# Kernel optimization log

Measured on AMD Instinct MI355X. Metric: run time of the kernel, lower is better.

Reference implementation:

```python
import jax, jax.numpy as jnp
import numpy as np

D_MODEL = 1024
N_HEADS = 16
D_K = D_MODEL // N_HEADS


def setup_inputs() -> dict:
    key = jax.random.key(0)
    k1, k2, k3, k4, k5 = jax.random.split(key, 5)
    B, S = 2, 2048
    scale = 1.0 / np.sqrt(D_MODEL)
    return {
        "query": jax.random.normal(k1, (B, S, D_MODEL), dtype=jnp.float32),
        "mask": jnp.ones((B, S, S), dtype=jnp.int32),
        "W_qkv": jax.random.normal(k2, (D_MODEL, 3 * D_MODEL), dtype=jnp.float32) * scale,
        "b_qkv": jax.random.normal(k3, (3 * D_MODEL,), dtype=jnp.float32) * 0.02,
        "W_out": jax.random.normal(k4, (D_MODEL, D_MODEL), dtype=jnp.float32) * scale,
        "b_out": jax.random.normal(k5, (D_MODEL,), dtype=jnp.float32) * 0.02,
    }


def reference(query, mask, W_qkv, b_qkv, W_out, b_out):
    B, S, _ = query.shape
    # fused QKV projection (all from query, matching the torch module)
    qkv = query @ W_qkv + b_qkv                      # [B, S, 3*D]
    q, k, v = jnp.split(qkv, 3, axis=-1)
    # [B, H, S, d_k]
    q = q.reshape(B, S, N_HEADS, D_K).transpose(0, 2, 1, 3)
    k = k.reshape(B, S, N_HEADS, D_K).transpose(0, 2, 1, 3)
    v = v.reshape(B, S, N_HEADS, D_K).transpose(0, 2, 1, 3)
    # scaled dot-product attention with explicit scores
    scores = jnp.einsum("bhqd,bhkd->bhqk", q, k) / jnp.sqrt(jnp.float32(D_K))
    m = mask[:, None, :, :]                           # [B, 1, S, S] broadcast over heads
    scores = jnp.where(m == 0, jnp.float32(-1e9), scores)
    attn = jax.nn.softmax(scores, axis=-1)           # dropout p=0 in eval -> identity
    ctx = jnp.einsum("bhqk,bhkd->bhqd", attn, v)     # [B, H, S, d_k]
    ctx = ctx.transpose(0, 2, 1, 3).reshape(B, S, D_MODEL)
    return ctx @ W_out + b_out
```

## Files before the change

kernel.cpp:

```cpp
#include <hip/hip_runtime.h>
#include <stdint.h>
#include <stddef.h>

#define S_LEN 2048
#define NB    2
#define DM    1024
#define NH    16
#define DKH   64
#define NTOK  4096
#define QKV_N 3072
#define QSCALE 0.18033688f

typedef __attribute__((ext_vector_type(4))) float floatx4;
using half2v = __attribute__((ext_vector_type(2))) _Float16;
using half4v = __attribute__((ext_vector_type(4))) _Float16;
using half8v = __attribute__((ext_vector_type(8))) _Float16;
using fp16x2 = __attribute__((ext_vector_type(2))) __fp16;

#if __has_builtin(__builtin_amdgcn_exp2f)
#define EXP2F __builtin_amdgcn_exp2f
#else
#define EXP2F exp2f
#endif

#define WAITCNT_VM4() asm volatile("s_waitcnt vmcnt(4)" ::: "memory")
#define WAITCNT_VM0() asm volatile("s_waitcnt vmcnt(0)" ::: "memory")
#define BARRIER_RAW() asm volatile("s_barrier" ::: "memory")

__device__ __forceinline__ void glds16(const void* g, void* l) {
    __builtin_amdgcn_global_load_lds((const __attribute__((address_space(1))) void*)g,
                                     (__attribute__((address_space(3))) void*)l,
                                     16, 0, 0);
}

__global__ __launch_bounds__(256) void prep_kernel(const float* __restrict__ query,
                                                   _Float16* __restrict__ qh,
                                                   const float* __restrict__ Wqkv,
                                                   _Float16* __restrict__ wqt,
                                                   const float* __restrict__ Wout,
                                                   _Float16* __restrict__ wot,
                                                   const int* __restrict__ mask,
                                                   int* __restrict__ flag) {
    __shared__ float tbuf[32][33];
    constexpr int CAST_B = NTOK * DM / 4 / 256;
    constexpr int TQ_B   = (QKV_N / 32) * (DM / 32);
    constexpr int TO_B   = (DM / 32) * (DM / 32);
    const int bid = blockIdx.x;

    if (bid < CAST_B) {
        int i = bid * 256 + threadIdx.x;
        float4 v = ((const float4*)query)[i];
        half4v o = {(_Float16)v.x, (_Float16)v.y, (_Float16)v.z, (_Float16)v.w};
        ((half4v*)qh)[i] = o;
    } else if (bid < CAST_B + TQ_B + TO_B) {
        const float* in; _Float16* out; int C, t;
        if (bid < CAST_B + TQ_B) { t = bid - CAST_B;        in = Wqkv; out = wqt; C = QKV_N; }
        else                     { t = bid - CAST_B - TQ_B; in = Wout; out = wot; C = DM;    }
        const int R = DM;
        int c0 = (t % (C / 32)) * 32, r0 = (t / (C / 32)) * 32;
        int x = threadIdx.x & 31, y0 = threadIdx.x >> 5;
        #pragma unroll
        for (int k = 0; k < 4; ++k) {
            int y = y0 + k * 8;
            tbuf[y][x] = in[(size_t)(r0 + y) * C + c0 + x];
        }
        __syncthreads();
        #pragma unroll
        for (int k = 0; k < 4; ++k) {
            int y = y0 + k * 8;
            out[(size_t)(c0 + y) * R + r0 + x] = (_Float16)tbuf[x][y];
        }
    } else {
        int i = (bid - CAST_B - TQ_B - TO_B) * 256 + threadIdx.x;
        int4 v = ((const int4*)mask)[i];
        if ((v.x == 0) | (v.y == 0) | (v.z == 0) | (v.w == 0)) *flag = 0;
    }
}

template <int FINAL, int BN>
__global__ __launch_bounds__(256) void gemm_bt_kernel(const _Float16* __restrict__ A,
                                                      const _Float16* __restrict__ Bt,
                                                      const float* __restrict__ bias,
                                                      float* __restrict__ Cf,
                                                      _Float16* __restrict__ Ch,
                                                      _Float16* __restrict__ Vt,
                                                      int M, int N, int K) {
    constexpr int NJ = BN / 32;
    __shared__ _Float16 As[128 * 64];
    __shared__ _Float16 Bs[BN * 64];

    const int nt = blockIdx.x, mt = blockIdx.y;
    const int tid = threadIdx.x, wave = tid >> 6, lane = tid & 63;
    const int quad = lane >> 4, l16 = lane & 15;
    const int wm = wave >> 1, wn = wave & 1;

    floatx4 acc[4][NJ];
    #pragma unroll
    for (int i = 0; i < 4; ++i)
        #pragma unroll
        for (int j = 0; j < NJ; ++j)
            #pragma unroll
            for (int r = 0; r < 4; ++r) acc[i][j][r] = 0.0f;

    const _Float16* Ab = A + (size_t)mt * 128 * K;
    const _Float16* Bb = Bt + (size_t)nt * BN * K;

    for (int kt = 0; kt < K; kt += 64) {
        #pragma unroll
        for (int p = 0; p < 4; ++p) {
            int slot = p * 256 + wave * 64 + lane;
            int row = slot >> 3, cc = slot & 7, c = cc ^ (row & 7);
            glds16(Ab + (size_t)row * K + kt + c * 8, As + (size_t)(p * 256 + wave * 64) * 8);
        }
        #pragma unroll
        for (int p = 0; p < BN / 32; ++p) {
            int slot = p * 256 + wave * 64 + lane;
            int row = slot >> 3, cc = slot & 7, c = cc ^ (row & 7);
            glds16(Bb + (size_t)row * K + kt + c * 8, Bs + (size_t)(p * 256 + wave * 64) * 8);
        }
        __syncthreads();

        #pragma unroll
        for (int kk = 0; kk < 2; ++kk) {
            half8v af[4], bfr[NJ];
            #pragma unroll
            for (int i = 0; i < 4; ++i) {
                int row = wm * 64 + i * 16 + l16;
                int c = (kk * 4 + quad) ^ (row & 7);
                af[i] = *(const half8v*)(As + row * 64 + c * 8);
            }
            #pragma unroll
            for (int j = 0; j < NJ; ++j) {
                int row = wn * (BN / 2) + j * 16 + l16;
                int c = (kk * 4 + quad) ^ (row & 7);
                bfr[j] = *(const half8v*)(Bs + row * 64 + c * 8);
            }
            #pragma unroll
            for (int i = 0; i < 4; ++i)
                #pragma unroll
                for (int j = 0; j < NJ; ++j)
                    acc[i][j] = __builtin_amdgcn_mfma_f32_16x16x32_f16(af[i], bfr[j], acc[i][j], 0, 0, 0);
        }
        __syncthreads();
    }

    #pragma unroll
    for (int j = 0; j < NJ; ++j) {
        int n = nt * BN + wn * (BN / 2) + j * 16 + l16;
        float bv = bias[n];
        #pragma unroll
        for (int i = 0; i < 4; ++i) {
            int m0 = mt * 128 + wm * 64 + i * 16 + quad * 4;
            float v[4];
            #pragma unroll
            for (int r = 0; r < 4; ++r) v[r] = acc[i][j][r] + bv;
            if (FINAL) {
                #pragma unroll
                for (int r = 0; r < 4; ++r) Cf[(size_t)(m0 + r) * N + n] = v[r];
            } else {
                if (n < DM) {
                    #pragma unroll
                    for (int r = 0; r < 4; ++r) v[r] *= QSCALE;
                }
                if (n < 2 * DM) {
                    #pragma unroll
                    for (int r = 0; r < 4; ++r)
                        Ch[(size_t)(m0 + r) * QKV_N + n] = (_Float16)v[r];
                } else {
                    int bb = m0 >> 11, s = m0 & (S_LEN - 1);
                    half4v t = {(_Float16)v[0], (_Float16)v[1], (_Float16)v[2], (_Float16)v[3]};
                    *(half4v*)(Vt + ((size_t)bb * (NH * DKH) + (n - 2 * DM)) * S_LEN + s) = t;
                }
            }
        }
    }
}

__global__ __launch_bounds__(512, 4) void flash_kernel(const _Float16* __restrict__ qkv,
                                                       const _Float16* __restrict__ vt,
                                                       const int* __restrict__ mask,
                                                       const int* __restrict__ flag,
                                                       _Float16* __restrict__ ctx) {
    __shared__ _Float16 Ks[2][2][64 * 64];
    __shared__ _Float16 Vs[2][2][64 * 64];

    const int bh = blockIdx.x, qt = blockIdx.y;
    const int b = bh >> 4, h = bh & 15;
    const int tid = threadIdx.x, wave = tid >> 6, lane = tid & 63;
    const int quad = lane >> 4, l16 = lane & 15;
    const int grp = wave >> 2;
    const int w4 = wave & 3;
    const int allones = (*flag != 0);

    const _Float16* qrow0 = qkv + (size_t)(b * S_LEN + qt * 128 + w4 * 32 + l16) * QKV_N + h * DKH;
    const _Float16* qrow1 = qrow0 + (size_t)16 * QKV_N;
    half8v qa0 = *(const half8v*)(qrow0 + quad * 8);
    half8v qa1 = *(const half8v*)(qrow0 + 32 + quad * 8);
    half8v qb0 = *(const half8v*)(qrow1 + quad * 8);
    half8v qb1 = *(const half8v*)(qrow1 + 32 + quad * 8);
    WAITCNT_VM0();

    const _Float16* kbase = qkv + (size_t)(b * S_LEN + grp * 1024) * QKV_N + DM + h * DKH;
    const _Float16* vbase = vt + (size_t)(b * NH + h) * DKH * S_LEN + grp * 1024;

    auto stage = [&](int buf, int kt) {
        #pragma unroll
        for (int p = 0; p < 2; ++p) {
            int slot = p * 256 + w4 * 64 + lane;
            int row = slot >> 3, cc = slot & 7, c = cc ^ (row & 7);
            glds16(kbase + (size_t)(kt * 64 + row) * QKV_N + c * 8,
                   &Ks[grp][buf][(p * 256 + w4 * 64) * 8]);
        }
        #pragma unroll
        for (int p = 0; p < 2; ++p) {
            int slot = p * 256 + w4 * 64 + lane;
            int row = slot >> 3, cc = slot & 7, c = cc ^ (row & 7);
            glds16(vbase + (size_t)row * S_LEN + kt * 64 + c * 8,
                   &Vs[grp][buf][(p * 256 + w4 * 64) * 8]);
        }
    };

    floatx4 oa[4], ob[4];
    #pragma unroll
    for (int c = 0; c < 4; ++c)
        #pragma unroll
        for (int r = 0; r < 4; ++r) { oa[c][r] = 0.0f; ob[c][r] = 0.0f; }
    float lsa = 0.0f, lsb = 0.0f;

    stage(0, 0);

    for (int kt = 0; kt < 16; ++kt) {
        const int cur = kt & 1;
        if (kt < 15) {
            stage(cur ^ 1, kt + 1);
            WAITCNT_VM4();
        } else {
            WAITCNT_VM0();
        }
        BARRIER_RAW();

        const _Float16* Ksb = Ks[grp][cur];
        const _Float16* Vsb = Vs[grp][cur];

        half4v pa[4], pb[4];
        #pragma unroll
        for (int j = 0; j < 4; ++j) {
            int rowk = j * 16 + l16;
            half8v a0 = *(const half8v*)(Ksb + rowk * 64 + ((quad) ^ (rowk & 7)) * 8);
            half8v a1 = *(const half8v*)(Ksb + rowk * 64 + ((4 + quad) ^ (rowk & 7)) * 8);
            floatx4 za, zb;
            #pragma unroll
            for (int r = 0; r < 4; ++r) { za[r] = 0.0f; zb[r] = 0.0f; }
            za = __builtin_amdgcn_mfma_f32_16x16x32_f16(a0, qa0, za, 0, 0, 0);
            za = __builtin_amdgcn_mfma_f32_16x16x32_f16(a1, qa1, za, 0, 0, 0);
            zb = __builtin_amdgcn_mfma_f32_16x16x32_f16(a0, qb0, zb, 0, 0, 0);
            zb = __builtin_amdgcn_mfma_f32_16x16x32_f16(a1, qb1, zb, 0, 0, 0);

            if (!allones) {
                for (int r = 0; r < 4; ++r) {
                    int s = grp * 1024 + kt * 64 + j * 16 + quad * 4 + r;
                    int qA = qt * 128 + w4 * 32 + l16;
                    if (mask[((size_t)b * S_LEN + qA) * S_LEN + s] == 0) za[r] = -1e9f;
                    if (mask[((size_t)b * S_LEN + qA + 16) * S_LEN + s] == 0) zb[r] = -1e9f;
                }
            }

            float p0 = EXP2F(za[0]), p1 = EXP2F(za[1]), p2 = EXP2F(za[2]), p3 = EXP2F(za[3]);
            lsa += (p0 + p1) + (p2 + p3);
            fp16x2 lo = __builtin_amdgcn_cvt_pkrtz(p0, p1);
            fp16x2 hi = __builtin_amdgcn_cvt_pkrtz(p2, p3);
            half2v lo2 = __builtin_bit_cast(half2v, lo);
            half2v hi2 = __builtin_bit_cast(half2v, hi);
            half4v pka = {lo2.x, lo2.y, hi2.x, hi2.y};
            pa[j] = pka;

            p0 = EXP2F(zb[0]); p1 = EXP2F(zb[1]); p2 = EXP2F(zb[2]); p3 = EXP2F(zb[3]);
            lsb += (p0 + p1) + (p2 + p3);
            lo = __builtin_amdgcn_cvt_pkrtz(p0, p1);
            hi = __builtin_amdgcn_cvt_pkrtz(p2, p3);
            lo2 = __builtin_bit_cast(half2v, lo);
            hi2 = __builtin_bit_cast(half2v, hi);
            half4v pkb = {lo2.x, lo2.y, hi2.x, hi2.y};
            pb[j] = pkb;
        }

        #pragma unroll
        for (int j = 0; j < 4; ++j) {
            int g2 = 2 * j + (quad >> 1);
            #pragma unroll
            for (int c = 0; c < 4; ++c) {
                int rowv = c * 16 + l16;
                half4v bv = *(const half4v*)(Vsb + rowv * 64 + ((g2 ^ (rowv & 7)) * 8) + (quad & 1) * 4);
                oa[c] = __builtin_amdgcn_mfma_f32_16x16x16f16(pa[j], bv, oa[c], 0, 0, 0);
                ob[c] = __builtin_amdgcn_mfma_f32_16x16x16f16(pb[j], bv, ob[c], 0, 0, 0);
            }
        }

        if (kt < 15) BARRIER_RAW();
    }

    __syncthreads();
    float* obuf = (float*)&Ks[0][0][0];
    float* lbuf = (float*)&Vs[0][0][0];
    if (grp == 1) {
        #pragma unroll
        for (int c = 0; c < 4; ++c)
            #pragma unroll
            for (int r = 0; r < 4; ++r) {
                obuf[(w4 * 32 + (c * 4 + r)) * 64 + lane]      = oa[c][r];
                obuf[(w4 * 32 + 16 + (c * 4 + r)) * 64 + lane] = ob[c][r];
            }
        lbuf[(w4 * 2 + 0) * 64 + lane] = lsa;
        lbuf[(w4 * 2 + 1) * 64 + lane] = lsb;
    }
    __syncthreads();
    if (grp == 0) {
        #pragma unroll
        for (int c = 0; c < 4; ++c)
            #pragma unroll
            for (int r = 0; r < 4; ++r) {
                oa[c][r] += obuf[(w4 * 32 + (c * 4 + r)) * 64 + lane];
                ob[c][r] += obuf[(w4 * 32 + 16 + (c * 4 + r)) * 64 + lane];
            }
        lsa += lbuf[(w4 * 2 + 0) * 64 + lane];
        lsb += lbuf[(w4 * 2 + 1) * 64 + lane];

        lsa += __shfl_xor(lsa, 16); lsa += __shfl_xor(lsa, 32);
        lsb += __shfl_xor(lsb, 16); lsb += __shfl_xor(lsb, 32);
        float lia[4], lib[4];
        #pragma unroll
        for (int r = 0; r < 4; ++r) {
            int src = (lane & 48) | ((lane >> 4) * 4 + r);
            lia[r] = 1.0f / __shfl(lsa, src);
            lib[r] = 1.0f / __shfl(lsb, src);
        }

        #pragma unroll
        for (int c = 0; c < 4; ++c)
            #pragma unroll
            for (int r = 0; r < 4; ++r) {
                int qA = qt * 128 + w4 * 32 + quad * 4 + r;
                int col = h * DKH + c * 16 + l16;
                ctx[(size_t)(b * S_LEN + qA) * DM + col]      = (_Float16)(oa[c][r] * lia[r]);
                ctx[(size_t)(b * S_LEN + qA + 16) * DM + col] = (_Float16)(ob[c][r] * lib[r]);
            }
    }
}

extern "C" void kernel_launch(void* const* d_in, const int* in_sizes, int n_in,
                              void* d_out, int out_size, void* d_ws, size_t ws_size,
                              hipStream_t stream) {
    const float* query = (const float*)d_in[0];
    const int*   mask  = (const int*)d_in[1];
    const float* W_qkv = (const float*)d_in[2];
    const float* b_qkv = (const float*)d_in[3];
    const float* W_out = (const float*)d_in[4];
    const float* b_out = (const float*)d_in[5];
    float* out = (float*)d_out;

    char* w = (char*)d_ws;
    _Float16* qh   = (_Float16*)w;  w += (size_t)NTOK * DM * 2;
    _Float16* wqt  = (_Float16*)w;  w += (size_t)QKV_N * DM * 2;
    _Float16* wot  = (_Float16*)w;  w += (size_t)DM * DM * 2;
    _Float16* qkvh = (_Float16*)w;  w += (size_t)NTOK * QKV_N * 2;
    _Float16* vt   = (_Float16*)w;  w += (size_t)NB * NH * DKH * S_LEN * 2;
    int*      flag = (int*)w;
    _Float16* ctxh = qh;

    hipMemsetAsync(flag, 1, 4, stream);

    constexpr int PREP_BLOCKS = (NTOK * DM / 4 / 256)
                              + (QKV_N / 32) * (DM / 32)
                              + (DM / 32) * (DM / 32)
                              + (NB * S_LEN * S_LEN / 4 / 256);
    prep_kernel<<<PREP_BLOCKS, 256, 0, stream>>>(query, qh, W_qkv, wqt, W_out, wot, mask, flag);

    gemm_bt_kernel<0, 128><<<dim3(QKV_N / 128, NTOK / 128), 256, 0, stream>>>(
        qh, wqt, b_qkv, nullptr, qkvh, vt, NTOK, QKV_N, DM);

    flash_kernel<<<dim3(NB * NH, S_LEN / 128), 512, 0, stream>>>(qkvh, vt, mask, flag, ctxh);

    gemm_bt_kernel<1, 64><<<dim3(DM / 64, NTOK / 128), 256, 0, stream>>>(
        ctxh, wot, b_out, out, nullptr, nullptr, NTOK, DM, DM);
}
```

Baseline: 211.2 us.

## Double-buffer GEMM K-tiles and stage attention output through LDS for coalesced stores

The GEMM kernel now uses two 32-wide K buffers in LDS and issues async global-to-LDS loads for the next tile before computing the current one, synchronising with vmcnt waits and raw barriers instead of two full __syncthreads per 64-wide step. It also sets launch_bounds occupancy to 4 blocks. The attention epilogue writes the normalized fp16 context into LDS first and then stores it to global memory as 16-byte coalesced rows instead of scattered 2-byte stores. The aim is to overlap memory latency with MFMA work and cut store transactions, at the cost of more barriers per K and possible register pressure from the occupancy hint.

New measurement: 218.4 us. +3.4%, slower.

```diff
diff --git a/kernel.cpp b/kernel.cpp
--- a/kernel.cpp
+++ b/kernel.cpp
@@ -24,6 +24,7 @@
 #endif
 
 #define WAITCNT_VM4() asm volatile("s_waitcnt vmcnt(4)" ::: "memory")
+#define WAITCNT_VM3() asm volatile("s_waitcnt vmcnt(3)" ::: "memory")
 #define WAITCNT_VM0() asm volatile("s_waitcnt vmcnt(0)" ::: "memory")
 #define BARRIER_RAW() asm volatile("s_barrier" ::: "memory")
 
@@ -78,16 +79,16 @@
 }
 
 template <int FINAL, int BN>
-__global__ __launch_bounds__(256) void gemm_bt_kernel(const _Float16* __restrict__ A,
-                                                      const _Float16* __restrict__ Bt,
-                                                      const float* __restrict__ bias,
-                                                      float* __restrict__ Cf,
-                                                      _Float16* __restrict__ Ch,
-                                                      _Float16* __restrict__ Vt,
-                                                      int M, int N, int K) {
+__global__ __launch_bounds__(256, 4) void gemm_bt_kernel(const _Float16* __restrict__ A,
+                                                         const _Float16* __restrict__ Bt,
+                                                         const float* __restrict__ bias,
+                                                         float* __restrict__ Cf,
+                                                         _Float16* __restrict__ Ch,
+                                                         _Float16* __restrict__ Vt,
+                                                         int M, int N, int K) {
     constexpr int NJ = BN / 32;
-    __shared__ _Float16 As[128 * 64];
-    __shared__ _Float16 Bs[BN * 64];
+    __shared__ _Float16 As[2][128 * 32];
+    __shared__ _Float16 Bs[2][BN * 32];
 
     const int nt = blockIdx.x, mt = blockIdx.y;
     const int tid = threadIdx.x, wave = tid >> 6, lane = tid & 63;
@@ -105,43 +106,53 @@
     const _Float16* Ab = A + (size_t)mt * 128 * K;
     const _Float16* Bb = Bt + (size_t)nt * BN * K;
 
-    for (int kt = 0; kt < K; kt += 64) {
-        #pragma unroll
-        for (int p = 0; p < 4; ++p) {
+    auto stage = [&](int buf, int kt) {
+        #pragma unroll
+        for (int p = 0; p < 2; ++p) {
             int slot = p * 256 + wave * 64 + lane;
-            int row = slot >> 3, cc = slot & 7, c = cc ^ (row & 7);
-            glds16(Ab + (size_t)row * K + kt + c * 8, As + (size_t)(p * 256 + wave * 64) * 8);
-        }
-        #pragma unroll
-        for (int p = 0; p < BN / 32; ++p) {
+            int row = slot >> 2, cc = slot & 3, c = cc ^ (row & 3);
+            glds16(Ab + (size_t)row * K + kt * 32 + c * 8, &As[buf][(p * 256 + wave * 64) * 8]);
+        }
+        #pragma unroll
+        for (int p = 0; p < BN / 64; ++p) {
             int slot = p * 256 + wave * 64 + lane;
-            int row = slot >> 3, cc = slot & 7, c = cc ^ (row & 7);
-            glds16(Bb + (size_t)row * K + kt + c * 8, Bs + (size_t)(p * 256 + wave * 64) * 8);
-        }
-        __syncthreads();
-
-        #pragma unroll
-        for (int kk = 0; kk < 2; ++kk) {
-            half8v af[4], bfr[NJ];
-            #pragma unroll
-            for (int i = 0; i < 4; ++i) {
-                int row = wm * 64 + i * 16 + l16;
-                int c = (kk * 4 + quad) ^ (row & 7);
-                af[i] = *(const half8v*)(As + row * 64 + c * 8);
-            }
-            #pragma unroll
-            for (int j = 0; j < NJ; ++j) {
-                int row = wn * (BN / 2) + j * 16 + l16;
-                int c = (kk * 4 + quad) ^ (row & 7);
-                bfr[j] = *(const half8v*)(Bs + row * 64 + c * 8);
-            }
-            #pragma unroll
-            for (int i = 0; i < 4; ++i)
-                #pragma unroll
-                for (int j = 0; j < NJ; ++j)
-                    acc[i][j] = __builtin_amdgcn_mfma_f32_16x16x32_f16(af[i], bfr[j], acc[i][j], 0, 0, 0);
-        }
-        __syncthreads();
+            int row = slot >> 2, cc = slot & 3, c = cc ^ (row & 3);
+            glds16(Bb + (size_t)row * K + kt * 32 + c * 8, &Bs[buf][(p * 256 + wave * 64) * 8]);
+        }
+    };
+
+    stage(0, 0);
+    const int NKT = K / 32;
+    for (int kt = 0; kt < NKT; ++kt) {
+        const int cur = kt & 1;
+        if (kt < NKT - 1) {
+            stage(cur ^ 1, kt + 1);
+            if constexpr (BN == 128) { WAITCNT_VM4(); } else { WAITCNT_VM3(); }
+        } else {
+            WAITCNT_VM0();
+        }
+        BARRIER_RAW();
+
+        half8v af[4], bfr[NJ];
+        #pragma unroll
+        for (int i = 0; i < 4; ++i) {
+            int row = wm * 64 + i * 16 + l16;
+            int c = quad ^ (row & 3);
+            af[i] = *(const half8v*)(&As[cur][row * 32 + c * 8]);
+        }
+        #pragma unroll
+        for (int j = 0; j < NJ; ++j) {
+            int row = wn * (BN / 2) + j * 16 + l16;
+            int c = quad ^ (row & 3);
+            bfr[j] = *(const half8v*)(&Bs[cur][row * 32 + c * 8]);
+        }
+        #pragma unroll
+        for (int i = 0; i < 4; ++i)
+            #pragma unroll
+            for (int j = 0; j < NJ; ++j)
+                acc[i][j] = __builtin_amdgcn_mfma_f32_16x16x32_f16(af[i], bfr[j], acc[i][j], 0, 0, 0);
+
+        if (kt < NKT - 1) BARRIER_RAW();
     }
 
     #pragma unroll
@@ -302,6 +313,7 @@
     __syncthreads();
     float* obuf = (float*)&Ks[0][0][0];
     float* lbuf = (float*)&Vs[0][0][0];
+    _Float16* st = (_Float16*)&Vs[0][0][0] + 2048;
     if (grp == 1) {
         #pragma unroll
         for (int c = 0; c < 4; ++c)
@@ -339,11 +351,18 @@
         for (int c = 0; c < 4; ++c)
             #pragma unroll
             for (int r = 0; r < 4; ++r) {
-                int qA = qt * 128 + w4 * 32 + quad * 4 + r;
-                int col = h * DKH + c * 16 + l16;
-                ctx[(size_t)(b * S_LEN + qA) * DM + col]      = (_Float16)(oa[c][r] * lia[r]);
-                ctx[(size_t)(b * S_LEN + qA + 16) * DM + col] = (_Float16)(ob[c][r] * lib[r]);
-            }
+                st[(w4 * 32 + quad * 4 + r) * 64 + c * 16 + l16]      = (_Float16)(oa[c][r] * lia[r]);
+                st[(w4 * 32 + 16 + quad * 4 + r) * 64 + c * 16 + l16] = (_Float16)(ob[c][r] * lib[r]);
+            }
+    }
+    __syncthreads();
+
+    #pragma unroll
+    for (int p = 0; p < 2; ++p) {
+        int cid = p * 512 + tid;
+        int row = cid >> 3, off = (cid & 7) * 8;
+        half8v vv = *(const half8v*)(st + row * 64 + off);
+        *(half8v*)(ctx + (size_t)(b * S_LEN + qt * 128 + row) * DM + h * DKH + off) = vv;
     }
 }
 
```

## Triple-buffer GEMM shared-memory tiles with async prefetch two stages ahead

Applied to the files above, without the earlier changes.

Turns the GEMM k-loop into a three-stage pipeline. global_load_lds copies for tile kt+2 are issued before computing tile kt, and explicit vmcnt waits plus raw barriers replace the load-then-sync pattern, so global memory latency overlaps with MFMA work. The K tile size becomes a template parameter: 32 for the QKV projection and 64 for the output projection. The cost is three times the LDS per block, which may cut occupancy, and more barriers per unit of work in the BK=32 case.

After: 209.6 us. About the same (-0.8%).

```diff
diff --git a/kernel.cpp b/kernel.cpp
--- a/kernel.cpp
+++ b/kernel.cpp
@@ -26,6 +26,15 @@
 #define WAITCNT_VM4() asm volatile("s_waitcnt vmcnt(4)" ::: "memory")
 #define WAITCNT_VM0() asm volatile("s_waitcnt vmcnt(0)" ::: "memory")
 #define BARRIER_RAW() asm volatile("s_barrier" ::: "memory")
+
+template <int N> __device__ __forceinline__ void waitcnt_vm() {
+    if constexpr (N == 0)       asm volatile("s_waitcnt vmcnt(0)" ::: "memory");
+    else if constexpr (N == 4)  asm volatile("s_waitcnt vmcnt(4)" ::: "memory");
+    else if constexpr (N == 6)  asm volatile("s_waitcnt vmcnt(6)" ::: "memory");
+    else if constexpr (N == 8)  asm volatile("s_waitcnt vmcnt(8)" ::: "memory");
+    else if constexpr (N == 12) asm volatile("s_waitcnt vmcnt(12)" ::: "memory");
+    else static_assert(N == 0, "unsupported vmcnt");
+}
 
 __device__ __forceinline__ void glds16(const void* g, void* l) {
     __builtin_amdgcn_global_load_lds((const __attribute__((address_space(1))) void*)g,
@@ -77,7 +86,7 @@
     }
 }
 
-template <int FINAL, int BN>
+template <int FINAL, int BN, int BK>
 __global__ __launch_bounds__(256) void gemm_bt_kernel(const _Float16* __restrict__ A,
                                                       const _Float16* __restrict__ Bt,
                                                       const float* __restrict__ bias,
@@ -85,9 +94,13 @@
                                                       _Float16* __restrict__ Ch,
                                                       _Float16* __restrict__ Vt,
                                                       int M, int N, int K) {
-    constexpr int NJ = BN / 32;
-    __shared__ _Float16 As[128 * 64];
-    __shared__ _Float16 Bs[BN * 64];
+    constexpr int NJ  = BN / 32;
+    constexpr int GR  = BK / 8;
+    constexpr int NKK = BK / 32;
+    constexpr int PA  = 128 * GR / 256;
+    constexpr int PB  = BN * GR / 256;
+    __shared__ _Float16 As[3][128 * BK];
+    __shared__ _Float16 Bs[3][BN * BK];
 
     const int nt = blockIdx.x, mt = blockIdx.y;
     const int tid = threadIdx.x, wave = tid >> 6, lane = tid & 63;
@@ -105,35 +118,53 @@
     const _Float16* Ab = A + (size_t)mt * 128 * K;
     const _Float16* Bb = Bt + (size_t)nt * BN * K;
 
-    for (int kt = 0; kt < K; kt += 64) {
-        #pragma unroll
-        for (int p = 0; p < 4; ++p) {
-            int slot = p * 256 + wave * 64 + lane;
-            int row = slot >> 3, cc = slot & 7, c = cc ^ (row & 7);
-            glds16(Ab + (size_t)row * K + kt + c * 8, As + (size_t)(p * 256 + wave * 64) * 8);
-        }
-        #pragma unroll
-        for (int p = 0; p < BN / 32; ++p) {
-            int slot = p * 256 + wave * 64 + lane;
-            int row = slot >> 3, cc = slot & 7, c = cc ^ (row & 7);
-            glds16(Bb + (size_t)row * K + kt + c * 8, Bs + (size_t)(p * 256 + wave * 64) * 8);
-        }
-        __syncthreads();
-
-        #pragma unroll
-        for (int kk = 0; kk < 2; ++kk) {
+    auto stage = [&](int buf, int kt) {
+        #pragma unroll
+        for (int p = 0; p < PA; ++p) {
+            int slot = p * 256 + tid;
+            int row = slot / GR, cc = slot % GR, c = cc ^ (row & (GR - 1));
+            glds16(Ab + (size_t)row * K + kt * BK + c * 8,
+                   &As[buf][(size_t)(p * 256 + wave * 64) * 8]);
+        }
+        #pragma unroll
+        for (int p = 0; p < PB; ++p) {
+            int slot = p * 256 + tid;
+            int row = slot / GR, cc = slot % GR, c = cc ^ (row & (GR - 1));
+            glds16(Bb + (size_t)row * K + kt * BK + c * 8,
+                   &Bs[buf][(size_t)(p * 256 + wave * 64) * 8]);
+        }
+    };
+
+    const int NKT = K / BK;
+    stage(0, 0);
+    stage(1, 1);
+
+    int cur = 0;
+    for (int kt = 0; kt < NKT; ++kt) {
+        if (kt + 2 < NKT) {
+            stage((kt + 2) % 3, kt + 2);
+            waitcnt_vm<2 * (PA + PB)>();
+        } else if (kt + 2 == NKT) {
+            waitcnt_vm<PA + PB>();
+        } else {
+            waitcnt_vm<0>();
+        }
+        BARRIER_RAW();
+
+        #pragma unroll
+        for (int kk = 0; kk < NKK; ++kk) {
             half8v af[4], bfr[NJ];
             #pragma unroll
             for (int i = 0; i < 4; ++i) {
                 int row = wm * 64 + i * 16 + l16;
-                int c = (kk * 4 + quad) ^ (row & 7);
-                af[i] = *(const half8v*)(As + row * 64 + c * 8);
+                int c = (kk * 4 + quad) ^ (row & (GR - 1));
+                af[i] = *(const half8v*)(&As[cur][row * BK + c * 8]);
             }
             #pragma unroll
             for (int j = 0; j < NJ; ++j) {
                 int row = wn * (BN / 2) + j * 16 + l16;
-                int c = (kk * 4 + quad) ^ (row & 7);
-                bfr[j] = *(const half8v*)(Bs + row * 64 + c * 8);
+                int c = (kk * 4 + quad) ^ (row & (GR - 1));
+                bfr[j] = *(const half8v*)(&Bs[cur][row * BK + c * 8]);
             }
             #pragma unroll
             for (int i = 0; i < 4; ++i)
@@ -141,7 +172,9 @@
                 for (int j = 0; j < NJ; ++j)
                     acc[i][j] = __builtin_amdgcn_mfma_f32_16x16x32_f16(af[i], bfr[j], acc[i][j], 0, 0, 0);
         }
-        __syncthreads();
+
+        if (kt < NKT - 1) BARRIER_RAW();
+        cur = (cur == 2) ? 0 : cur + 1;
     }
 
     #pragma unroll
@@ -375,11 +408,11 @@
                               + (NB * S_LEN * S_LEN / 4 / 256);
     prep_kernel<<<PREP_BLOCKS, 256, 0, stream>>>(query, qh, W_qkv, wqt, W_out, wot, mask, flag);
 
-    gemm_bt_kernel<0, 128><<<dim3(QKV_N / 128, NTOK / 128), 256, 0, stream>>>(
+    gemm_bt_kernel<0, 128, 32><<<dim3(QKV_N / 128, NTOK / 128), 256, 0, stream>>>(
         qh, wqt, b_qkv, nullptr, qkvh, vt, NTOK, QKV_N, DM);
 
     flash_kernel<<<dim3(NB * NH, S_LEN / 128), 512, 0, stream>>>(qkvh, vt, mask, flag, ctxh);
 
-    gemm_bt_kernel<1, 64><<<dim3(DM / 64, NTOK / 128), 256, 0, stream>>>(
+    gemm_bt_kernel<1, 64, 64><<<dim3(DM / 64, NTOK / 128), 256, 0, stream>>>(
         ctxh, wot, b_out, out, nullptr, nullptr, NTOK, DM, DM);
 }
```

## Overlap mask scan and W_out transpose with QKV GEMM via interleaved blocks

Applied to the files above, without the earlier changes.

Moves the mask scan and the W_out transpose/cast out of the prep kernel and into the QKV projection GEMM launch. One in every 13 blocks does a GEMM tile and the other 12 do mask or transpose work, so the memory-bound side work can run alongside the MFMA-bound GEMM. This shortens the critical prep kernel, but the GEMM grid becomes sparse and interleaved, which may change scheduling and cache behavior. The block counts must match exactly: 12 side blocks per GEMM tile times 768 tiles must cover all mask and transpose blocks.

Result: slower. 216.6 us (+2.5%).

```diff
diff --git a/kernel.cpp b/kernel.cpp
--- a/kernel.cpp
+++ b/kernel.cpp
@@ -36,15 +36,9 @@
 __global__ __launch_bounds__(256) void prep_kernel(const float* __restrict__ query,
                                                    _Float16* __restrict__ qh,
                                                    const float* __restrict__ Wqkv,
-                                                   _Float16* __restrict__ wqt,
-                                                   const float* __restrict__ Wout,
-                                                   _Float16* __restrict__ wot,
-                                                   const int* __restrict__ mask,
-                                                   int* __restrict__ flag) {
+                                                   _Float16* __restrict__ wqt) {
     __shared__ float tbuf[32][33];
     constexpr int CAST_B = NTOK * DM / 4 / 256;
-    constexpr int TQ_B   = (QKV_N / 32) * (DM / 32);
-    constexpr int TO_B   = (DM / 32) * (DM / 32);
     const int bid = blockIdx.x;
 
     if (bid < CAST_B) {
@@ -52,39 +46,161 @@
         float4 v = ((const float4*)query)[i];
         half4v o = {(_Float16)v.x, (_Float16)v.y, (_Float16)v.z, (_Float16)v.w};
         ((half4v*)qh)[i] = o;
-    } else if (bid < CAST_B + TQ_B + TO_B) {
-        const float* in; _Float16* out; int C, t;
-        if (bid < CAST_B + TQ_B) { t = bid - CAST_B;        in = Wqkv; out = wqt; C = QKV_N; }
-        else                     { t = bid - CAST_B - TQ_B; in = Wout; out = wot; C = DM;    }
-        const int R = DM;
+    } else {
+        int t = bid - CAST_B;
+        const int C = QKV_N, R = DM;
         int c0 = (t % (C / 32)) * 32, r0 = (t / (C / 32)) * 32;
         int x = threadIdx.x & 31, y0 = threadIdx.x >> 5;
         #pragma unroll
         for (int k = 0; k < 4; ++k) {
             int y = y0 + k * 8;
-            tbuf[y][x] = in[(size_t)(r0 + y) * C + c0 + x];
+            tbuf[y][x] = query == nullptr ? 0.f : Wqkv[(size_t)(r0 + y) * C + c0 + x];
         }
         __syncthreads();
         #pragma unroll
         for (int k = 0; k < 4; ++k) {
             int y = y0 + k * 8;
-            out[(size_t)(c0 + y) * R + r0 + x] = (_Float16)tbuf[x][y];
-        }
-    } else {
-        int i = (bid - CAST_B - TQ_B - TO_B) * 256 + threadIdx.x;
-        int4 v = ((const int4*)mask)[i];
-        if ((v.x == 0) | (v.y == 0) | (v.z == 0) | (v.w == 0)) *flag = 0;
-    }
-}
-
-template <int FINAL, int BN>
-__global__ __launch_bounds__(256) void gemm_bt_kernel(const _Float16* __restrict__ A,
-                                                      const _Float16* __restrict__ Bt,
-                                                      const float* __restrict__ bias,
-                                                      float* __restrict__ Cf,
-                                                      _Float16* __restrict__ Ch,
-                                                      _Float16* __restrict__ Vt,
-                                                      int M, int N, int K) {
+            wqt[(size_t)(c0 + y) * R + r0 + x] = (_Float16)tbuf[x][y];
+        }
+    }
+}
+
+__global__ __launch_bounds__(256) void gemm1_fused_kernel(const _Float16* __restrict__ A,
+                                                          const _Float16* __restrict__ Bt,
+                                                          const float* __restrict__ bias,
+                                                          _Float16* __restrict__ Ch,
+                                                          _Float16* __restrict__ Vt,
+                                                          const float* __restrict__ Wout,
+                                                          _Float16* __restrict__ wot,
+                                                          const int* __restrict__ mask,
+                                                          int* __restrict__ flag) {
+    constexpr int BN = 128, NJ = BN / 32;
+    constexpr int MASK_B = NB * S_LEN * S_LEN / 4 / 256;
+    constexpr int TO_B   = (DM / 32) * (DM / 32);
+    constexpr int NTGRID = QKV_N / 128;
+    __shared__ _Float16 As[128 * 64];
+    __shared__ _Float16 Bs[BN * 64];
+
+    const int bid = blockIdx.x;
+    const int tid = threadIdx.x;
+
+    if (bid % 13 != 0) {
+        int a = bid - bid / 13 - 1;
+        if (a < MASK_B) {
+            int i = a * 256 + tid;
+            int4 v = ((const int4*)mask)[i];
+            if ((v.x == 0) | (v.y == 0) | (v.z == 0) | (v.w == 0)) *flag = 0;
+        } else {
+            int t = a - MASK_B;
+            float* tb = (float*)As;
+            const int C = DM, R = DM;
+            int c0 = (t % 32) * 32, r0 = (t / 32) * 32;
+            int x = tid & 31, y0 = tid >> 5;
+            #pragma unroll
+            for (int k = 0; k < 4; ++k) {
+                int y = y0 + k * 8;
+                tb[y * 33 + x] = Wout[(size_t)(r0 + y) * C + c0 + x];
+            }
+            __syncthreads();
+            #pragma unroll
+            for (int k = 0; k < 4; ++k) {
+                int y = y0 + k * 8;
+                wot[(size_t)(c0 + y) * R + r0 + x] = (_Float16)tb[x * 33 + y];
+            }
+        }
+        return;
+    }
+
+    const int r = bid / 13;
+    const int nt = r % NTGRID, mt = r / NTGRID;
+    const int wave = tid >> 6, lane = tid & 63;
+    const int quad = lane >> 4, l16 = lane & 15;
+    const int wm = wave >> 1, wn = wave & 1;
+    const int M = NTOK, N = QKV_N, K = DM;
+
+    floatx4 acc[4][NJ];
+    #pragma unroll
+    for (int i = 0; i < 4; ++i)
+        #pragma unroll
+        for (int j = 0; j < NJ; ++j)
+            #pragma unroll
+            for (int rr = 0; rr < 4; ++rr) acc[i][j][rr] = 0.0f;
+
+    const _Float16* Ab = A + (size_t)mt * 128 * K;
+    const _Float16* Bb = Bt + (size_t)nt * BN * K;
+
+    for (int kt = 0; kt < K; kt += 64) {
+        #pragma unroll
+        for (int p = 0; p < 4; ++p) {
+            int slot = p * 256 + wave * 64 + lane;
+            int row = slot >> 3, cc = slot & 7, c = cc ^ (row & 7);
+            glds16(Ab + (size_t)row * K + kt + c * 8, As + (size_t)(p * 256 + wave * 64) * 8);
+        }
+        #pragma unroll
+        for (int p = 0; p < BN / 32; ++p) {
+            int slot = p * 256 + wave * 64 + lane;
+            int row = slot >> 3, cc = slot & 7, c = cc ^ (row & 7);
+            glds16(Bb + (size_t)row * K + kt + c * 8, Bs + (size_t)(p * 256 + wave * 64) * 8);
+        }
+        __syncthreads();
+
+        #pragma unroll
+        for (int kk = 0; kk < 2; ++kk) {
+            half8v af[4], bfr[NJ];
+            #pragma unroll
+            for (int i = 0; i < 4; ++i) {
+                int row = wm * 64 + i * 16 + l16;
+                int c = (kk * 4 + quad) ^ (row & 7);
+                af[i] = *(const half8v*)(As + row * 64 + c * 8);
+            }
+            #pragma unroll
+            for (int j = 0; j < NJ; ++j) {
+                int row = wn * (BN / 2) + j * 16 + l16;
+                int c = (kk * 4 + quad) ^ (row & 7);
+                bfr[j] = *(const half8v*)(Bs + row * 64 + c * 8);
+            }
+            #pragma unroll
+            for (int i = 0; i < 4; ++i)
+                #pragma unroll
+                for (int j = 0; j < NJ; ++j)
+                    acc[i][j] = __builtin_amdgcn_mfma_f32_16x16x32_f16(af[i], bfr[j], acc[i][j], 0, 0, 0);
+        }
+        __syncthreads();
+    }
+
+    #pragma unroll
+    for (int j = 0; j < NJ; ++j) {
+        int n = nt * BN + wn * (BN / 2) + j * 16 + l16;
+        float bv = bias[n];
+        #pragma unroll
+        for (int i = 0; i < 4; ++i) {
+            int m0 = mt * 128 + wm * 64 + i * 16 + quad * 4;
+            float v[4];
+            #pragma unroll
+            for (int rr = 0; rr < 4; ++rr) v[rr] = acc[i][j][rr] + bv;
+            if (n < DM) {
+                #pragma unroll
+                for (int rr = 0; rr < 4; ++rr) v[rr] *= QSCALE;
+            }
+            if (n < 2 * DM) {
+                #pragma unroll
+                for (int rr = 0; rr < 4; ++rr)
+                    Ch[(size_t)(m0 + rr) * QKV_N + n] = (_Float16)v[rr];
+            } else {
+                int bb = m0 >> 11, s = m0 & (S_LEN - 1);
+                half4v t = {(_Float16)v[0], (_Float16)v[1], (_Float16)v[2], (_Float16)v[3]};
+                *(half4v*)(Vt + ((size_t)bb * (NH * DKH) + (n - 2 * DM)) * S_LEN + s) = t;
+            }
+        }
+    }
+}
+
+template <int BN>
+__global__ __launch_bounds__(256) void gemm2_kernel(const _Float16* __restrict__ A,
+                                                    const _Float16* __restrict__ Bt,
+                                                    const float* __restrict__ bias,
+                                                    float* __restrict__ Cf,
+                                                    int M, int N, int K) {
     constexpr int NJ = BN / 32;
     __shared__ _Float16 As[128 * 64];
     __shared__ _Float16 Bs[BN * 64];
@@ -151,27 +267,8 @@
         #pragma unroll
         for (int i = 0; i < 4; ++i) {
             int m0 = mt * 128 + wm * 64 + i * 16 + quad * 4;
-            float v[4];
-            #pragma unroll
-            for (int r = 0; r < 4; ++r) v[r] = acc[i][j][r] + bv;
-            if (FINAL) {
-                #pragma unroll
-                for (int r = 0; r < 4; ++r) Cf[(size_t)(m0 + r) * N + n] = v[r];
-            } else {
-                if (n < DM) {
-                    #pragma unroll
-                    for (int r = 0; r < 4; ++r) v[r] *= QSCALE;
-                }
-                if (n < 2 * DM) {
-                    #pragma unroll
-                    for (int r = 0; r < 4; ++r)
-                        Ch[(size_t)(m0 + r) * QKV_N + n] = (_Float16)v[r];
-                } else {
-                    int bb = m0 >> 11, s = m0 & (S_LEN - 1);
-                    half4v t = {(_Float16)v[0], (_Float16)v[1], (_Float16)v[2], (_Float16)v[3]};
-                    *(half4v*)(Vt + ((size_t)bb * (NH * DKH) + (n - 2 * DM)) * S_LEN + s) = t;
-                }
-            }
+            #pragma unroll
+            for (int r = 0; r < 4; ++r) Cf[(size_t)(m0 + r) * N + n] = acc[i][j][r] + bv;
         }
     }
 }
@@ -370,16 +467,15 @@
     hipMemsetAsync(flag, 1, 4, stream);
 
     constexpr int PREP_BLOCKS = (NTOK * DM / 4 / 256)
-                              + (QKV_N / 32) * (DM / 32)
-                              + (DM / 32) * (DM / 32)
-                              + (NB * S_LEN * S_LEN / 4 / 256);
-    prep_kernel<<<PREP_BLOCKS, 256, 0, stream>>>(query, qh, W_qkv, wqt, W_out, wot, mask, flag);
-
-    gemm_bt_kernel<0, 128><<<dim3(QKV_N / 128, NTOK / 128), 256, 0, stream>>>(
-        qh, wqt, b_qkv, nullptr, qkvh, vt, NTOK, QKV_N, DM);
+                              + (QKV_N / 32) * (DM / 32);
+    prep_kernel<<<PREP_BLOCKS, 256, 0, stream>>>(query, qh, W_qkv, wqt);
+
+    constexpr int G1_BLOCKS = 13 * (QKV_N / 128) * (NTOK / 128);
+    gemm1_fused_kernel<<<G1_BLOCKS, 256, 0, stream>>>(
+        qh, wqt, b_qkv, qkvh, vt, W_out, wot, mask, flag);
 
     flash_kernel<<<dim3(NB * NH, S_LEN / 128), 512, 0, stream>>>(qkvh, vt, mask, flag, ctxh);
 
-    gemm_bt_kernel<1, 64><<<dim3(DM / 64, NTOK / 128), 256, 0, stream>>>(
-        ctxh, wot, b_out, out, nullptr, nullptr, NTOK, DM, DM);
-}
+    gemm2_kernel<64><<<dim3(DM / 64, NTOK / 128), 256, 0, stream>>>(
+        ctxh, wot, b_out, out, NTOK, DM, DM);
+}
```
